# Kernel optimization log

Hardware: AMD Instinct MI355X
Metric: run time of the kernel (lower is better)

The kernel has to match this reference:

```python
import jax, jax.numpy as jnp
import numpy as np

B, SQ, SK, H, NH = 2, 2048, 2048, 1024, 16
HD = H // NH  # 64


def setup_inputs() -> dict:
    key = jax.random.key(0)
    ks = jax.random.split(key, 12)
    s = 1.0 / np.sqrt(H)
    inp = {
        "query": jax.random.normal(ks[0], (B, SQ, H), jnp.float32),
        "key": jax.random.normal(ks[1], (B, SK, H), jnp.float32),
        "value": jax.random.normal(ks[2], (B, SK, H), jnp.float32),
        # lower-triangular causal mask [B, SQ, SK]; nonzero = attend
        "causal_mask": jnp.broadcast_to(
            jnp.tril(jnp.ones((SQ, SK), jnp.int32)), (B, SQ, SK)
        ),
        "Wq": jax.random.uniform(ks[3], (H, H), jnp.float32, -s, s),
        "bq": jnp.zeros((H,), jnp.float32),
        "Wk": jax.random.uniform(ks[4], (H, H), jnp.float32, -s, s),
        "bk": jnp.zeros((H,), jnp.float32),
        "Wv": jax.random.uniform(ks[5], (H, H), jnp.float32, -s, s),
        "bv": jnp.zeros((H,), jnp.float32),
        "Wo": jax.random.uniform(ks[6], (H, H), jnp.float32, -s, s),
        "bo": jnp.zeros((H,), jnp.float32),
        "ln_g": jnp.ones((H,), jnp.float32),
        "ln_b": jnp.zeros((H,), jnp.float32),
    }
    return inp


def _layer_norm(x, g, b, eps=1e-5):
    mu = jnp.mean(x, axis=-1, keepdims=True)
    var = jnp.var(x, axis=-1, keepdims=True)
    return (x - mu) * jax.lax.rsqrt(var + eps) * g + b


def reference(query, key, value, causal_mask, Wq, bq, Wk, bk, Wv, bv, Wo, bo, ln_g, ln_b):
    # projections (torch Linear: x @ W.T + b)
    q = (query @ Wq.T + bq).reshape(B, SQ, NH, HD)
    k = (key @ Wk.T + bk).reshape(B, SK, NH, HD)
    v = (value @ Wv.T + bv).reshape(B, SK, NH, HD)
    # scores [B, NH, SQ, SK]
    scores = jnp.einsum("bqhd,bkhd->bhqk", q, k) / np.sqrt(HD).astype(np.float32)
    scores = jnp.where(causal_mask[:, None, :, :] == 0, -jnp.inf, scores)
    attn = jax.nn.softmax(scores, axis=-1)
    # dropout is identity in eval mode
    out = jnp.einsum("bhqk,bkhd->bqhd", attn, v).reshape(B, SQ, H)
    out = out @ Wo.T + bo
    return _layer_norm(query + out, ln_g, ln_b)
```

## Files before the change

### kernel.cpp

```cpp
#include <hip/hip_runtime.h>
#include <hip/hip_bf16.h>

#define SQL 2048
#define SKL 2048
#define HH  1024
#define NHH 16
#define HDD 64
#define BB  2
#define MM  (BB*SQL)

typedef __attribute__((ext_vector_type(8))) short short8;
typedef __attribute__((ext_vector_type(4))) short short4v;
typedef __attribute__((ext_vector_type(4))) float f32x4;
typedef unsigned short u16;

__device__ inline u16 f2bf(float f) {
    unsigned int u = __float_as_uint(f);
    u += 0x7fffu + ((u >> 16) & 1u);
    return (u16)(u >> 16);
}

__device__ inline void gl_lds16(const void* g, void* l) {
    __builtin_amdgcn_global_load_lds(
        (const __attribute__((address_space(1))) unsigned int*)g,
        (__attribute__((address_space(3))) unsigned int*)l, 16, 0, 0);
}

__global__ __launch_bounds__(256) void cvt_all_kernel(
    const float* __restrict__ q, const float* __restrict__ k, const float* __restrict__ v,
    const float* __restrict__ wq, const float* __restrict__ wk,
    const float* __restrict__ wv, const float* __restrict__ wo,
    u16* __restrict__ xq, u16* __restrict__ xk, u16* __restrict__ xv,
    u16* __restrict__ wqb, u16* __restrict__ wkb, u16* __restrict__ wvb, u16* __restrict__ wob)
{
    int b = blockIdx.x;
    const float* src; u16* dst;
    if      (b < 4096)  { src = q;  dst = xq; }
    else if (b < 8192)  { src = k;  dst = xk;  b -= 4096; }
    else if (b < 12288) { src = v;  dst = xv;  b -= 8192; }
    else if (b < 13312) { src = wq; dst = wqb; b -= 12288; }
    else if (b < 14336) { src = wk; dst = wkb; b -= 13312; }
    else if (b < 15360) { src = wv; dst = wvb; b -= 14336; }
    else                { src = wo; dst = wob; b -= 15360; }
    int i = (b * 256 + threadIdx.x) * 4;
    float4 vv = *(const float4*)(src + i);
    ushort4 oo;
    oo.x = f2bf(vv.x); oo.y = f2bf(vv.y); oo.z = f2bf(vv.z); oo.w = f2bf(vv.w);
    *(ushort4*)(dst + i) = oo;
}

__global__ __launch_bounds__(256) void proj_kernel(
    const u16* __restrict__ xq, const u16* __restrict__ xk, const u16* __restrict__ xv,
    const u16* __restrict__ wqb, const u16* __restrict__ wkb, const u16* __restrict__ wvb,
    const float* __restrict__ bq, const float* __restrict__ bk, const float* __restrict__ bv,
    u16* __restrict__ oq, u16* __restrict__ ok, u16* __restrict__ ov)
{
    const int z = blockIdx.z;
    const u16* A      = (z == 0) ? xq  : (z == 1) ? xk  : xv;
    const u16* W      = (z == 0) ? wqb : (z == 1) ? wkb : wvb;
    const float* bias = (z == 0) ? bq  : (z == 1) ? bk  : bv;
    u16* outb         = (z == 0) ? oq  : (z == 1) ? ok  : ov;
    const float scale = (z == 0) ? 0.125f * 1.4426950408889634f : 1.0f;

    __shared__ u16 lds_a[2][128 * 32];
    __shared__ u16 lds_b[2][128 * 32];

    const int t = threadIdx.x;
    const int lane = t & 63;
    const int quad = lane >> 4;
    const int lo = lane & 15;
    const int wv = t >> 6;
    const int wm = (wv >> 1) * 64, wn = (wv & 1) * 64;
    const int m0 = blockIdx.x * 128;
    const int n0 = blockIdx.y * 128;

    f32x4 acc[4][4];
#pragma unroll
    for (int i = 0; i < 4; i++)
#pragma unroll
        for (int j = 0; j < 4; j++) acc[i][j] = (f32x4){0.f, 0.f, 0.f, 0.f};

    const int sl0 = t, sl1 = 256 + t;
    const int r0 = sl0 >> 2, c0 = ((sl0 & 3) ^ ((r0 >> 1) & 3)) * 8;
    const int r1 = sl1 >> 2, c1 = ((sl1 & 3) ^ ((r1 >> 1) & 3)) * 8;

    gl_lds16(A + (size_t)(m0 + r0) * HH + c0, &lds_a[0][sl0 * 8]);
    gl_lds16(A + (size_t)(m0 + r1) * HH + c1, &lds_a[0][sl1 * 8]);
    gl_lds16(W + (size_t)(n0 + r0) * HH + c0, &lds_b[0][sl0 * 8]);
    gl_lds16(W + (size_t)(n0 + r1) * HH + c1, &lds_b[0][sl1 * 8]);
    __syncthreads();

    int cur = 0;
    for (int k0 = 0; k0 < HH; k0 += 32) {
        if (k0 + 32 < HH) {
            const int kn = k0 + 32;
            gl_lds16(A + (size_t)(m0 + r0) * HH + kn + c0, &lds_a[cur ^ 1][sl0 * 8]);
            gl_lds16(A + (size_t)(m0 + r1) * HH + kn + c1, &lds_a[cur ^ 1][sl1 * 8]);
            gl_lds16(W + (size_t)(n0 + r0) * HH + kn + c0, &lds_b[cur ^ 1][sl0 * 8]);
            gl_lds16(W + (size_t)(n0 + r1) * HH + kn + c1, &lds_b[cur ^ 1][sl1 * 8]);
        }
        short8 af[4], bf[4];
#pragma unroll
        for (int i = 0; i < 4; i++) {
            const int ra = wm + i * 16 + lo;
            const int rb = wn + i * 16 + lo;
            af[i] = *(const short8*)&lds_a[cur][ra * 32 + ((quad ^ ((ra >> 1) & 3)) * 8)];
            bf[i] = *(const short8*)&lds_b[cur][rb * 32 + ((quad ^ ((rb >> 1) & 3)) * 8)];
        }
        if (z == 2) {
#pragma unroll
            for (int i = 0; i < 4; i++)
#pragma unroll
                for (int j = 0; j < 4; j++)
                    acc[i][j] = __builtin_amdgcn_mfma_f32_16x16x32_bf16(bf[j], af[i], acc[i][j], 0, 0, 0);
        } else {
#pragma unroll
            for (int i = 0; i < 4; i++)
#pragma unroll
                for (int j = 0; j < 4; j++)
                    acc[i][j] = __builtin_amdgcn_mfma_f32_16x16x32_bf16(af[i], bf[j], acc[i][j], 0, 0, 0);
        }
        __syncthreads();
        cur ^= 1;
    }

#pragma unroll
    for (int i = 0; i < 4; i++) {
#pragma unroll
        for (int j = 0; j < 4; j++) {
#pragma unroll
            for (int r = 0; r < 4; r++) {
                if (z == 2) {
                    int dg  = n0 + wn + j * 16 + quad * 4 + r;
                    int tok = m0 + wm + i * 16 + lo;
                    float val = acc[i][j][r] + bias[dg];
                    int head = dg >> 6, d = dg & 63;
                    int bi = tok >> 11, s = tok & 2047;
                    outb[(((size_t)bi * NHH + head) * HDD + d) * SKL + s] = f2bf(val);
                } else {
                    int row = m0 + wm + i * 16 + quad * 4 + r;
                    int col = n0 + wn + j * 16 + lo;
                    float val = (acc[i][j][r] + bias[col]) * scale;
                    int bi = row >> 11, s = row & 2047;
                    int head = col >> 6, d = col & 63;
                    outb[(((size_t)bi * NHH + head) * SQL + s) * HDD + d] = f2bf(val);
                }
            }
        }
    }
}

__global__ __launch_bounds__(256) void outproj_kernel(
    const u16* __restrict__ A, const u16* __restrict__ W,
    const float* __restrict__ bias, const float* __restrict__ resid,
    float* __restrict__ outf)
{
    __shared__ u16 lds_a[2][128 * 32];
    __shared__ u16 lds_b[2][128 * 32];

    const int t = threadIdx.x;
    const int lane = t & 63;
    const int quad = lane >> 4;
    const int lo = lane & 15;
    const int wv = t >> 6;
    const int wm = (wv >> 1) * 64, wn = (wv & 1) * 64;
    const int m0 = blockIdx.x * 128;
    const int n0 = blockIdx.y * 128;

    f32x4 acc[4][4];
#pragma unroll
    for (int i = 0; i < 4; i++)
#pragma unroll
        for (int j = 0; j < 4; j++) acc[i][j] = (f32x4){0.f, 0.f, 0.f, 0.f};

    const int sl0 = t, sl1 = 256 + t;
    const int r0 = sl0 >> 2, c0 = ((sl0 & 3) ^ ((r0 >> 1) & 3)) * 8;
    const int r1 = sl1 >> 2, c1 = ((sl1 & 3) ^ ((r1 >> 1) & 3)) * 8;

    gl_lds16(A + (size_t)(m0 + r0) * HH + c0, &lds_a[0][sl0 * 8]);
    gl_lds16(A + (size_t)(m0 + r1) * HH + c1, &lds_a[0][sl1 * 8]);
    gl_lds16(W + (size_t)(n0 + r0) * HH + c0, &lds_b[0][sl0 * 8]);
    gl_lds16(W + (size_t)(n0 + r1) * HH + c1, &lds_b[0][sl1 * 8]);
    __syncthreads();

    int cur = 0;
    for (int k0 = 0; k0 < HH; k0 += 32) {
        if (k0 + 32 < HH) {
            const int kn = k0 + 32;
            gl_lds16(A + (size_t)(m0 + r0) * HH + kn + c0, &lds_a[cur ^ 1][sl0 * 8]);
            gl_lds16(A + (size_t)(m0 + r1) * HH + kn + c1, &lds_a[cur ^ 1][sl1 * 8]);
            gl_lds16(W + (size_t)(n0 + r0) * HH + kn + c0, &lds_b[cur ^ 1][sl0 * 8]);
            gl_lds16(W + (size_t)(n0 + r1) * HH + kn + c1, &lds_b[cur ^ 1][sl1 * 8]);
        }
        short8 af[4], bf[4];
#pragma unroll
        for (int i = 0; i < 4; i++) {
            const int ra = wm + i * 16 + lo;
            const int rb = wn + i * 16 + lo;
            af[i] = *(const short8*)&lds_a[cur][ra * 32 + ((quad ^ ((ra >> 1) & 3)) * 8)];
            bf[i] = *(const short8*)&lds_b[cur][rb * 32 + ((quad ^ ((rb >> 1) & 3)) * 8)];
        }
#pragma unroll
        for (int i = 0; i < 4; i++)
#pragma unroll
            for (int j = 0; j < 4; j++)
                acc[i][j] = __builtin_amdgcn_mfma_f32_16x16x32_bf16(af[i], bf[j], acc[i][j], 0, 0, 0);
        __syncthreads();
        cur ^= 1;
    }

#pragma unroll
    for (int i = 0; i < 4; i++)
#pragma unroll
        for (int j = 0; j < 4; j++)
#pragma unroll
            for (int r = 0; r < 4; r++) {
                int row = m0 + wm + i * 16 + quad * 4 + r;
                int col = n0 + wn + j * 16 + lo;
                float val = acc[i][j][r] + bias[col] + resid[(size_t)row * HH + col];
                outf[(size_t)row * HH + col] = val;
            }
}

#define PSTR 72

__global__ __launch_bounds__(256) void attn_kernel(
    const u16* __restrict__ qb, const u16* __restrict__ kb, const u16* __restrict__ vtb,
    u16* __restrict__ attn_out)
{
    __shared__ u16 k_lds[64 * 64];
    __shared__ u16 vt_lds[64 * 64];
    __shared__ u16 p_lds[4 * 16 * PSTR];

    const int t = threadIdx.x;
    const int lane = t & 63;
    const int quad = lane >> 4;
    const int lo = lane & 15;
    const int w = t >> 6;
    const int qt = (SQL / 64 - 1) - (blockIdx.x >> 5);
    const int bh = blockIdx.x & 31;
    const int q0 = qt * 64;

    const u16* qbase = qb + ((size_t)bh * SQL + q0 + w * 16 + lo) * HDD + quad * 8;
    short8 qf0 = *(const short8*)qbase;
    short8 qf1 = *(const short8*)(qbase + 32);

    float m_s = -__builtin_inff(), l_s = 0.f;
    f32x4 o[4];
#pragma unroll
    for (int j = 0; j < 4; j++) o[j] = (f32x4){0.f, 0.f, 0.f, 0.f};

    const int sl0 = t, sl1 = 256 + t;
    const int r0 = sl0 >> 3, c0 = ((sl0 & 7) ^ (r0 & 7)) * 8;
    const int r1 = sl1 >> 3, c1 = ((sl1 & 7) ^ (r1 & 7)) * 8;
    const u16* kbh = kb + (size_t)bh * SKL * HDD;
    const u16* vbh = vtb + (size_t)bh * HDD * SKL;
    u16* ppriv = &p_lds[w * 16 * PSTR];

    for (int kt = 0; kt <= qt; kt++) {
        const int k0 = kt * 64;
        gl_lds16(kbh + (size_t)(k0 + r0) * HDD + c0, &k_lds[sl0 * 8]);
        gl_lds16(kbh + (size_t)(k0 + r1) * HDD + c1, &k_lds[sl1 * 8]);
        gl_lds16(vbh + (size_t)r0 * SKL + k0 + c0, &vt_lds[sl0 * 8]);
        gl_lds16(vbh + (size_t)r1 * SKL + k0 + c1, &vt_lds[sl1 * 8]);
        __syncthreads();

        f32x4 s[4];
        __builtin_amdgcn_s_setprio(1);
#pragma unroll
        for (int nt = 0; nt < 4; nt++) {
            const int row = nt * 16 + lo;
            short8 kf0 = *(const short8*)&k_lds[row * 64 + ((quad ^ (row & 7)) * 8)];
            short8 kf1 = *(const short8*)&k_lds[row * 64 + (((4 + quad) ^ (row & 7)) * 8)];
            s[nt] = (f32x4){0.f, 0.f, 0.f, 0.f};
            s[nt] = __builtin_amdgcn_mfma_f32_16x16x32_bf16(kf0, qf0, s[nt], 0, 0, 0);
            s[nt] = __builtin_amdgcn_mfma_f32_16x16x32_bf16(kf1, qf1, s[nt], 0, 0, 0);
        }
        __builtin_amdgcn_s_setprio(0);
        if (kt == qt) {
            const int ql = w * 16 + lo;
#pragma unroll
            for (int nt = 0; nt < 4; nt++)
#pragma unroll
                for (int r = 0; r < 4; r++)
                    if (nt * 16 + quad * 4 + r > ql) s[nt][r] = -__builtin_inff();
        }

        float mx = s[0][0];
#pragma unroll
        for (int nt = 0; nt < 4; nt++)
#pragma unroll
            for (int r = 0; r < 4; r++) mx = fmaxf(mx, s[nt][r]);
        mx = fmaxf(mx, __shfl_xor(mx, 16));
        mx = fmaxf(mx, __shfl_xor(mx, 32));

        if (!__all(mx - m_s <= 8.0f)) {
            float mnew = fmaxf(m_s, mx);
            float al = __builtin_amdgcn_exp2f(m_s - mnew);
            m_s = mnew;
            l_s *= al;
            float alr[4];
#pragma unroll
            for (int r = 0; r < 4; r++) alr[r] = __shfl(al, quad * 4 + r, 16);
#pragma unroll
            for (int nt = 0; nt < 4; nt++)
#pragma unroll
                for (int r = 0; r < 4; r++) o[nt][r] *= alr[r];
        }

        float rs = 0.f;
#pragma unroll
        for (int nt = 0; nt < 4; nt++)
#pragma unroll
            for (int r = 0; r < 4; r++) {
                s[nt][r] = __builtin_amdgcn_exp2f(s[nt][r] - m_s);
                rs += s[nt][r];
            }
        rs += __shfl_xor(rs, 16);
        rs += __shfl_xor(rs, 32);
        l_s += rs;

#pragma unroll
        for (int nt = 0; nt < 4; nt++) {
            short4v pk;
#pragma unroll
            for (int r = 0; r < 4; r++) pk[r] = (short)f2bf(s[nt][r]);
            *(short4v*)&ppriv[lo * PSTR + nt * 16 + quad * 4] = pk;
        }
        short8 pf0 = *(const short8*)&ppriv[lo * PSTR + quad * 8];
        short8 pf1 = *(const short8*)&ppriv[lo * PSTR + 32 + quad * 8];

        __builtin_amdgcn_s_setprio(1);
#pragma unroll
        for (int nt = 0; nt < 4; nt++) {
            const int row = nt * 16 + lo;
            short8 vf0 = *(const short8*)&vt_lds[row * 64 + ((quad ^ (row & 7)) * 8)];
            short8 vf1 = *(const short8*)&vt_lds[row * 64 + (((4 + quad) ^ (row & 7)) * 8)];
            o[nt] = __builtin_amdgcn_mfma_f32_16x16x32_bf16(pf0, vf0, o[nt], 0, 0, 0);
            o[nt] = __builtin_amdgcn_mfma_f32_16x16x32_bf16(pf1, vf1, o[nt], 0, 0, 0);
        }
        __builtin_amdgcn_s_setprio(0);
        __syncthreads();
    }

    const int b = bh >> 4, h = bh & 15;
    float inv[4];
#pragma unroll
    for (int r = 0; r < 4; r++) inv[r] = 1.0f / __shfl(l_s, quad * 4 + r, 16);
#pragma unroll
    for (int nt = 0; nt < 4; nt++)
#pragma unroll
        for (int r = 0; r < 4; r++) {
            int srow = q0 + w * 16 + quad * 4 + r;
            attn_out[((size_t)b * SQL + srow) * HH + h * HDD + nt * 16 + lo] =
                f2bf(o[nt][r] * inv[r]);
        }
}

__global__ __launch_bounds__(256) void ln_kernel(const float* __restrict__ x,
                                                 const float* __restrict__ g,
                                                 const float* __restrict__ bb,
                                                 float* __restrict__ out)
{
    const int row = blockIdx.x;
    const int t = threadIdx.x;
    const float* xr = x + (size_t)row * HH;
    float4 v = *(const float4*)(xr + t * 4);
    float s1 = v.x + v.y + v.z + v.w;
    float s2 = v.x * v.x + v.y * v.y + v.z * v.z + v.w * v.w;
#pragma unroll
    for (int off = 32; off; off >>= 1) { s1 += __shfl_xor(s1, off); s2 += __shfl_xor(s2, off); }
    __shared__ float red[8];
    if ((t & 63) == 0) { red[(t >> 6) * 2] = s1; red[(t >> 6) * 2 + 1] = s2; }
    __syncthreads();
    s1 = red[0] + red[2] + red[4] + red[6];
    s2 = red[1] + red[3] + red[5] + red[7];
    float mu = s1 * (1.0f / HH);
    float var = s2 * (1.0f / HH) - mu * mu;
    float rstd = rsqrtf(var + 1e-5f);
    float4 gg = *(const float4*)(g + t * 4);
    float4 b4 = *(const float4*)(bb + t * 4);
    float4 o;
    o.x = (v.x - mu) * rstd * gg.x + b4.x;
    o.y = (v.y - mu) * rstd * gg.y + b4.y;
    o.z = (v.z - mu) * rstd * gg.z + b4.z;
    o.w = (v.w - mu) * rstd * gg.w + b4.w;
    *(float4*)(out + (size_t)row * HH + t * 4) = o;
}

extern "C" void kernel_launch(void* const* d_in, const int* in_sizes, int n_in,
                              void* d_out, int out_size, void* d_ws, size_t ws_size,
                              hipStream_t stream)
{
    const float* query = (const float*)d_in[0];
    const float* key   = (const float*)d_in[1];
    const float* value = (const float*)d_in[2];
    const float* Wq = (const float*)d_in[4];
    const float* bq = (const float*)d_in[5];
    const float* Wk = (const float*)d_in[6];
    const float* bk = (const float*)d_in[7];
    const float* Wv = (const float*)d_in[8];
    const float* bv = (const float*)d_in[9];
    const float* Wo = (const float*)d_in[10];
    const float* bo = (const float*)d_in[11];
    const float* ln_g = (const float*)d_in[12];
    const float* ln_b = (const float*)d_in[13];
    float* out = (float*)d_out;

    char* wp = (char*)d_ws;
    auto alloc = [&](size_t bytes) { void* p = (void*)wp; wp += (bytes + 255) & ~(size_t)255; return p; };
    const int nW = HH * HH;
    const int nX = MM * HH;
    u16* wqb = (u16*)alloc((size_t)nW * 2);
    u16* wkb = (u16*)alloc((size_t)nW * 2);
    u16* wvb = (u16*)alloc((size_t)nW * 2);
    u16* wob = (u16*)alloc((size_t)nW * 2);
    u16* xq  = (u16*)alloc((size_t)nX * 2);
    u16* xk  = (u16*)alloc((size_t)nX * 2);
    u16* xv  = (u16*)alloc((size_t)nX * 2);
    u16* qbuf = (u16*)alloc((size_t)nX * 2);
    u16* kbuf = (u16*)alloc((size_t)nX * 2);
    u16* vbuf = (u16*)alloc((size_t)nX * 2);
    u16* attnb = (u16*)alloc((size_t)nX * 2);
    float* projf = (float*)alloc((size_t)nX * 4);

    cvt_all_kernel<<<16384, 256, 0, stream>>>(query, key, value, Wq, Wk, Wv, Wo,
                                              xq, xk, xv, wqb, wkb, wvb, wob);

    proj_kernel<<<dim3(32, 8, 3), 256, 0, stream>>>(
        xq, xk, xv, wqb, wkb, wvb, bq, bk, bv, qbuf, kbuf, vbuf);

    attn_kernel<<<1024, 256, 0, stream>>>(qbuf, kbuf, vbuf, attnb);

    outproj_kernel<<<dim3(32, 8), 256, 0, stream>>>(attnb, wob, bo, query, projf);

    ln_kernel<<<MM, 256, 0, stream>>>(projf, ln_g, ln_b, out);
}
```

Measured before the change: 294.0 us.

## Replace double-buffered K=32 GEMM tiles with single-buffered K=64 tiles

Both projection GEMM kernels now load a 128x64 K-slice per iteration into a single LDS buffer, using an 8-way XOR swizzle, instead of double-buffering 128x32 slices. This halves the number of loop iterations and barriers, and each load batch now feeds two MFMA sub-steps. The cost is that global-to-LDS loads no longer overlap with MFMA work, so every iteration waits for its loads to finish.

```diff
diff --git a/kernel.cpp b/kernel.cpp
--- a/kernel.cpp
+++ b/kernel.cpp
@@ -62,8 +62,8 @@
     u16* outb         = (z == 0) ? oq  : (z == 1) ? ok  : ov;
     const float scale = (z == 0) ? 0.125f * 1.4426950408889634f : 1.0f;
 
-    __shared__ u16 lds_a[2][128 * 32];
-    __shared__ u16 lds_b[2][128 * 32];
+    __shared__ u16 lds_a[128 * 64];
+    __shared__ u16 lds_b[128 * 64];
 
     const int t = threadIdx.x;
     const int lane = t & 63;
@@ -80,48 +80,46 @@
 #pragma unroll
         for (int j = 0; j < 4; j++) acc[i][j] = (f32x4){0.f, 0.f, 0.f, 0.f};
 
-    const int sl0 = t, sl1 = 256 + t;
-    const int r0 = sl0 >> 2, c0 = ((sl0 & 3) ^ ((r0 >> 1) & 3)) * 8;
-    const int r1 = sl1 >> 2, c1 = ((sl1 & 3) ^ ((r1 >> 1) & 3)) * 8;
-
-    gl_lds16(A + (size_t)(m0 + r0) * HH + c0, &lds_a[0][sl0 * 8]);
-    gl_lds16(A + (size_t)(m0 + r1) * HH + c1, &lds_a[0][sl1 * 8]);
-    gl_lds16(W + (size_t)(n0 + r0) * HH + c0, &lds_b[0][sl0 * 8]);
-    gl_lds16(W + (size_t)(n0 + r1) * HH + c1, &lds_b[0][sl1 * 8]);
-    __syncthreads();
-
-    int cur = 0;
-    for (int k0 = 0; k0 < HH; k0 += 32) {
-        if (k0 + 32 < HH) {
-            const int kn = k0 + 32;
-            gl_lds16(A + (size_t)(m0 + r0) * HH + kn + c0, &lds_a[cur ^ 1][sl0 * 8]);
-            gl_lds16(A + (size_t)(m0 + r1) * HH + kn + c1, &lds_a[cur ^ 1][sl1 * 8]);
-            gl_lds16(W + (size_t)(n0 + r0) * HH + kn + c0, &lds_b[cur ^ 1][sl0 * 8]);
-            gl_lds16(W + (size_t)(n0 + r1) * HH + kn + c1, &lds_b[cur ^ 1][sl1 * 8]);
-        }
-        short8 af[4], bf[4];
-#pragma unroll
-        for (int i = 0; i < 4; i++) {
-            const int ra = wm + i * 16 + lo;
-            const int rb = wn + i * 16 + lo;
-            af[i] = *(const short8*)&lds_a[cur][ra * 32 + ((quad ^ ((ra >> 1) & 3)) * 8)];
-            bf[i] = *(const short8*)&lds_b[cur][rb * 32 + ((quad ^ ((rb >> 1) & 3)) * 8)];
-        }
-        if (z == 2) {
-#pragma unroll
-            for (int i = 0; i < 4; i++)
-#pragma unroll
-                for (int j = 0; j < 4; j++)
-                    acc[i][j] = __builtin_amdgcn_mfma_f32_16x16x32_bf16(bf[j], af[i], acc[i][j], 0, 0, 0);
-        } else {
-#pragma unroll
-            for (int i = 0; i < 4; i++)
-#pragma unroll
-                for (int j = 0; j < 4; j++)
-                    acc[i][j] = __builtin_amdgcn_mfma_f32_16x16x32_bf16(af[i], bf[j], acc[i][j], 0, 0, 0);
-        }
-        __syncthreads();
-        cur ^= 1;
+    int rr[4], cc[4];
+#pragma unroll
+    for (int u = 0; u < 4; u++) {
+        int sl = u * 256 + t;
+        rr[u] = sl >> 3;
+        cc[u] = ((sl & 7) ^ (rr[u] & 7)) * 8;
+    }
+
+    for (int k0 = 0; k0 < HH; k0 += 64) {
+#pragma unroll
+        for (int u = 0; u < 4; u++) {
+            gl_lds16(A + (size_t)(m0 + rr[u]) * HH + k0 + cc[u], &lds_a[(u * 256 + t) * 8]);
+            gl_lds16(W + (size_t)(n0 + rr[u]) * HH + k0 + cc[u], &lds_b[(u * 256 + t) * 8]);
+        }
+        __syncthreads();
+#pragma unroll
+        for (int kk = 0; kk < 2; kk++) {
+            short8 af[4], bf[4];
+#pragma unroll
+            for (int i = 0; i < 4; i++) {
+                const int ra = wm + i * 16 + lo;
+                const int rb = wn + i * 16 + lo;
+                af[i] = *(const short8*)&lds_a[ra * 64 + (((kk * 4 + quad) ^ (ra & 7)) * 8)];
+                bf[i] = *(const short8*)&lds_b[rb * 64 + (((kk * 4 + quad) ^ (rb & 7)) * 8)];
+            }
+            if (z == 2) {
+#pragma unroll
+                for (int i = 0; i < 4; i++)
+#pragma unroll
+                    for (int j = 0; j < 4; j++)
+                        acc[i][j] = __builtin_amdgcn_mfma_f32_16x16x32_bf16(bf[j], af[i], acc[i][j], 0, 0, 0);
+            } else {
+#pragma unroll
+                for (int i = 0; i < 4; i++)
+#pragma unroll
+                    for (int j = 0; j < 4; j++)
+                        acc[i][j] = __builtin_amdgcn_mfma_f32_16x16x32_bf16(af[i], bf[j], acc[i][j], 0, 0, 0);
+            }
+        }
+        __syncthreads();
     }
 
 #pragma unroll
@@ -155,8 +153,8 @@
     const float* __restrict__ bias, const float* __restrict__ resid,
     float* __restrict__ outf)
 {
-    __shared__ u16 lds_a[2][128 * 32];
-    __shared__ u16 lds_b[2][128 * 32];
+    __shared__ u16 lds_a[128 * 64];
+    __shared__ u16 lds_b[128 * 64];
 
     const int t = threadIdx.x;
     const int lane = t & 63;
@@ -173,40 +171,38 @@
 #pragma unroll
         for (int j = 0; j < 4; j++) acc[i][j] = (f32x4){0.f, 0.f, 0.f, 0.f};
 
-    const int sl0 = t, sl1 = 256 + t;
-    const int r0 = sl0 >> 2, c0 = ((sl0 & 3) ^ ((r0 >> 1) & 3)) * 8;
-    const int r1 = sl1 >> 2, c1 = ((sl1 & 3) ^ ((r1 >> 1) & 3)) * 8;
-
-    gl_lds16(A + (size_t)(m0 + r0) * HH + c0, &lds_a[0][sl0 * 8]);
-    gl_lds16(A + (size_t)(m0 + r1) * HH + c1, &lds_a[0][sl1 * 8]);
-    gl_lds16(W + (size_t)(n0 + r0) * HH + c0, &lds_b[0][sl0 * 8]);
-    gl_lds16(W + (size_t)(n0 + r1) * HH + c1, &lds_b[0][sl1 * 8]);
-    __syncthreads();
-
-    int cur = 0;
-    for (int k0 = 0; k0 < HH; k0 += 32) {
-        if (k0 + 32 < HH) {
-            const int kn = k0 + 32;
-            gl_lds16(A + (size_t)(m0 + r0) * HH + kn + c0, &lds_a[cur ^ 1][sl0 * 8]);
-            gl_lds16(A + (size_t)(m0 + r1) * HH + kn + c1, &lds_a[cur ^ 1][sl1 * 8]);
-            gl_lds16(W + (size_t)(n0 + r0) * HH + kn + c0, &lds_b[cur ^ 1][sl0 * 8]);
-            gl_lds16(W + (size_t)(n0 + r1) * HH + kn + c1, &lds_b[cur ^ 1][sl1 * 8]);
-        }
-        short8 af[4], bf[4];
-#pragma unroll
-        for (int i = 0; i < 4; i++) {
-            const int ra = wm + i * 16 + lo;
-            const int rb = wn + i * 16 + lo;
-            af[i] = *(const short8*)&lds_a[cur][ra * 32 + ((quad ^ ((ra >> 1) & 3)) * 8)];
-            bf[i] = *(const short8*)&lds_b[cur][rb * 32 + ((quad ^ ((rb >> 1) & 3)) * 8)];
-        }
-#pragma unroll
-        for (int i = 0; i < 4; i++)
-#pragma unroll
-            for (int j = 0; j < 4; j++)
-                acc[i][j] = __builtin_amdgcn_mfma_f32_16x16x32_bf16(af[i], bf[j], acc[i][j], 0, 0, 0);
-        __syncthreads();
-        cur ^= 1;
+    int rr[4], cc[4];
+#pragma unroll
+    for (int u = 0; u < 4; u++) {
+        int sl = u * 256 + t;
+        rr[u] = sl >> 3;
+        cc[u] = ((sl & 7) ^ (rr[u] & 7)) * 8;
+    }
+
+    for (int k0 = 0; k0 < HH; k0 += 64) {
+#pragma unroll
+        for (int u = 0; u < 4; u++) {
+            gl_lds16(A + (size_t)(m0 + rr[u]) * HH + k0 + cc[u], &lds_a[(u * 256 + t) * 8]);
+            gl_lds16(W + (size_t)(n0 + rr[u]) * HH + k0 + cc[u], &lds_b[(u * 256 + t) * 8]);
+        }
+        __syncthreads();
+#pragma unroll
+        for (int kk = 0; kk < 2; kk++) {
+            short8 af[4], bf[4];
+#pragma unroll
+            for (int i = 0; i < 4; i++) {
+                const int ra = wm + i * 16 + lo;
+                const int rb = wn + i * 16 + lo;
+                af[i] = *(const short8*)&lds_a[ra * 64 + (((kk * 4 + quad) ^ (ra & 7)) * 8)];
+                bf[i] = *(const short8*)&lds_b[rb * 64 + (((kk * 4 + quad) ^ (rb & 7)) * 8)];
+            }
+#pragma unroll
+            for (int i = 0; i < 4; i++)
+#pragma unroll
+                for (int j = 0; j < 4; j++)
+                    acc[i][j] = __builtin_amdgcn_mfma_f32_16x16x32_bf16(af[i], bf[j], acc[i][j], 0, 0, 0);
+        }
+        __syncthreads();
     }
 
 #pragma unroll
```

After: 269.8 us. 8.2% less time.
